# Optimization experiments

Hardware: AMD Instinct MI355X
Metric: run time of the kernel (lower is better)

The kernel has to match this reference:

```python
import jax, jax.numpy as jnp
import numpy as np
from jax import lax

DN = ('NCHW', 'OIHW', 'NCHW')

def binarize(w):
    # torch: w.sign().add(0.5).sign() maps w<0 -> -1, w>=0 -> +1 (0 -> +1)
    return jnp.where(w < 0, -1.0, 1.0).astype(w.dtype)

def bconv(x, w, b, dil):
    wb = binarize(w)
    y = lax.conv_general_dilated(x, wb, window_strides=(1, 1), padding='SAME',
                                 rhs_dilation=dil, dimension_numbers=DN)
    return y + b[None, :, None, None]

def setup_inputs() -> dict:
    key = jax.random.key(0)
    ks = jax.random.split(key, 9)
    C = 256
    Co = C // 4
    x = jax.random.normal(ks[0], (16, C, 128, 128), dtype=jnp.float32)
    w1 = jax.random.normal(ks[1], (Co, C, 1, 5), dtype=jnp.float32) * 0.05
    w2 = jax.random.normal(ks[2], (Co, C, 1, 5), dtype=jnp.float32) * 0.05
    w3 = jax.random.normal(ks[3], (Co, C, 5, 1), dtype=jnp.float32) * 0.05
    w4 = jax.random.normal(ks[4], (Co, C, 5, 1), dtype=jnp.float32) * 0.05
    b1 = jax.random.normal(ks[5], (Co,), dtype=jnp.float32) * 0.01
    b2 = jax.random.normal(ks[6], (Co,), dtype=jnp.float32) * 0.01
    b3 = jax.random.normal(ks[7], (Co,), dtype=jnp.float32) * 0.01
    b4 = jax.random.normal(ks[8], (Co,), dtype=jnp.float32) * 0.01
    return {'x': x, 'w1': w1, 'b1': b1, 'w2': w2, 'b2': b2,
            'w3': w3, 'b3': b3, 'w4': w4, 'b4': b4}

def reference(x, w1, b1, w2, b2, w3, b3, w4, b4):
    out1 = bconv(x, w1, b1, (1, 1))  # (1,5) dil 1
    out2 = bconv(x, w2, b2, (2, 2))  # (1,5) dil 2 (only W dim matters, H kernel=1)
    out3 = bconv(x, w3, b3, (1, 1))  # (5,1) dil 1
    out4 = bconv(x, w4, b4, (2, 2))  # (5,1) dil 2
    return jnp.concatenate([out1, out2, out3, out4], axis=1)
```

## Files before the change

kernel.cpp:

```cpp
#include <hip/hip_runtime.h>

typedef _Float16 half8  __attribute__((ext_vector_type(8)));
typedef float    floatx4 __attribute__((ext_vector_type(4)));

#define HW      128
#define CIN     256
#define NCHUNK  8
#define HALO_W  24
#define HALO_H  16
#define PITCH   20

__global__ void prep_weights(const float* __restrict__ w1,
                             const float* __restrict__ w2,
                             const float* __restrict__ w3,
                             const float* __restrict__ w4,
                             _Float16* __restrict__ wp)
{
    int idx  = blockIdx.x * 256 + threadIdx.x;
    int ci   = idx & 255;
    int rest = idx >> 8;
    int co   = rest & 63;
    int bt   = rest >> 6;
    int t    = bt % 5;
    int b    = bt / 5;
    const float* w = (b == 0) ? w1 : (b == 1) ? w2 : (b == 2) ? w3 : w4;
    float v = w[(co * 256 + ci) * 5 + t];
    wp[idx] = (v < 0.0f) ? (_Float16)(-1.0f) : (_Float16)(1.0f);
}

__global__ __launch_bounds__(256, 2)
void bconv_mfma(const float* __restrict__ x,
                const _Float16* __restrict__ wp,
                const float* __restrict__ bb1,
                const float* __restrict__ bb2,
                const float* __restrict__ bb3,
                const float* __restrict__ bb4,
                float* __restrict__ out)
{
    __shared__ __align__(16) unsigned int xs[HALO_H * HALO_W * PITCH];
    __shared__ float bias_s[256];

    const int tid  = threadIdx.x;
    const int w0t  = blockIdx.x * 16;
    const int h0t  = blockIdx.y * 8;
    const int nimg = blockIdx.z;

    {
        int br = tid >> 6, i = tid & 63;
        const float* bp = (br == 0) ? bb1 : (br == 1) ? bb2 : (br == 2) ? bb3 : bb4;
        bias_s[tid] = bp[i];
    }

    const int lane = tid & 63;
    const int wave = tid >> 6;
    const int quad = lane >> 4;
    const int wl   = lane & 15;

    floatx4 acc[4][8];
    #pragma unroll
    for (int m = 0; m < 4; ++m)
        #pragma unroll
        for (int n = 0; n < 8; ++n)
            acc[m][n] = (floatx4){0.f, 0.f, 0.f, 0.f};

    const int  dil   = (wave & 1) + 1;
    const bool horiz = (wave < 2);

    for (int chunk = 0; chunk < NCHUNK; ++chunk) {
        __syncthreads();

        #pragma unroll
        for (int s = 0; s < 6; ++s) {
            int u   = s * 256 + tid;
            int f   = u % 6;
            int g   = u / 6;
            int hh  = g & 15;
            int cp  = g >> 4;
            int ci0 = chunk * 32 + cp * 2;
            int hg  = h0t - 4 + hh;
            int wg  = w0t - 4 + f * 4;
            floatx4 v0 = {0.f,0.f,0.f,0.f}, v1 = {0.f,0.f,0.f,0.f};
            if (hg >= 0 && hg < HW && wg >= 0 && wg <= HW - 4) {
                const floatx4* p = (const floatx4*)(x + ((nimg * CIN + ci0) * HW + hg) * HW + wg);
                v0 = p[0];
                v1 = p[(HW * HW) / 4];
            }
            int pixb = hh * HALO_W + f * 4;
            #pragma unroll
            for (int i = 0; i < 4; ++i) {
                xs[(pixb + i) * PITCH + cp] =
                    __builtin_bit_cast(unsigned int,
                        __builtin_amdgcn_cvt_pkrtz(v0[i], v1[i]));
            }
        }
        __syncthreads();

        #pragma unroll
        for (int t = 0; t < 5; ++t) {
            half8 B[8];
            #pragma unroll
            for (int n = 0; n < 8; ++n) {
                int hh, ww;
                if (horiz) { hh = n + 4;                  ww = wl + 4 + (t - 2) * dil; }
                else       { hh = n + 4 + (t - 2) * dil;  ww = wl + 4; }
                B[n] = *(const half8*)&xs[(hh * HALO_W + ww) * PITCH + quad * 4];
            }
            #pragma unroll
            for (int m = 0; m < 4; ++m) {
                half8 A = *(const half8*)(wp +
                    (((wave * 5 + t) * 64 + m * 16 + wl) * 256 + chunk * 32 + quad * 8));
                #pragma unroll
                for (int n = 0; n < 8; ++n)
                    acc[m][n] = __builtin_amdgcn_mfma_f32_16x16x32_f16(A, B[n], acc[m][n], 0, 0, 0);
            }
        }
    }

    float bv[4][4];
    #pragma unroll
    for (int m = 0; m < 4; ++m)
        #pragma unroll
        for (int r = 0; r < 4; ++r)
            bv[m][r] = bias_s[wave * 64 + m * 16 + quad * 4 + r];

    #pragma unroll
    for (int m = 0; m < 4; ++m) {
        #pragma unroll
        for (int n = 0; n < 8; ++n) {
            int co   = wave * 64 + m * 16 + quad * 4;
            int base = ((nimg * 256 + co) * HW + (h0t + n)) * HW + w0t + wl;
            #pragma unroll
            for (int r = 0; r < 4; ++r)
                out[base + r * HW * HW] = acc[m][n][r] + bv[m][r];
        }
    }
}

extern "C" void kernel_launch(void* const* d_in, const int* in_sizes, int n_in,
                              void* d_out, int out_size, void* d_ws, size_t ws_size,
                              hipStream_t stream)
{
    (void)in_sizes; (void)n_in; (void)out_size; (void)ws_size;
    const float* x  = (const float*)d_in[0];
    const float* w1 = (const float*)d_in[1];
    const float* b1 = (const float*)d_in[2];
    const float* w2 = (const float*)d_in[3];
    const float* b2 = (const float*)d_in[4];
    const float* w3 = (const float*)d_in[5];
    const float* b3 = (const float*)d_in[6];
    const float* w4 = (const float*)d_in[7];
    const float* b4 = (const float*)d_in[8];
    float*    out = (float*)d_out;
    _Float16* wp  = (_Float16*)d_ws;

    prep_weights<<<1280, 256, 0, stream>>>(w1, w2, w3, w4, wp);

    dim3 grid(128 / 16, 128 / 8, 16);
    bconv_mfma<<<grid, dim3(256), 0, stream>>>(x, wp, b1, b2, b3, b4, out);
}
```

Baseline: 671.4 us.

## Double-buffer input halo in LDS and repack weights for coalesced loads

```diff
diff --git a/kernel.cpp b/kernel.cpp
--- a/kernel.cpp
+++ b/kernel.cpp
@@ -1,13 +1,15 @@
 #include <hip/hip_runtime.h>
 
-typedef _Float16 half8  __attribute__((ext_vector_type(8)));
+typedef _Float16 half8   __attribute__((ext_vector_type(8)));
 typedef float    floatx4 __attribute__((ext_vector_type(4)));
+typedef unsigned int uint4v __attribute__((ext_vector_type(4)));
 
 #define HW      128
 #define CIN     256
 #define NCHUNK  8
 #define HALO_W  24
 #define HALO_H  16
+#define NPIX    (HALO_W * HALO_H)
 #define PITCH   20
 
 __global__ void prep_weights(const float* __restrict__ w1,
@@ -17,13 +19,17 @@
                              _Float16* __restrict__ wp)
 {
     int idx  = blockIdx.x * 256 + threadIdx.x;
-    int ci   = idx & 255;
-    int rest = idx >> 8;
-    int co   = rest & 63;
-    int bt   = rest >> 6;
-    int t    = bt % 5;
-    int b    = bt / 5;
+    int j    = idx & 7;
+    int lane = (idx >> 3) & 63;
+    int m    = (idx >> 9) & 3;
+    int r3   = idx >> 11;
+    int t    = r3 % 5;
+    int r4   = r3 / 5;
+    int chunk= r4 & 7;
+    int b    = r4 >> 3;
     const float* w = (b == 0) ? w1 : (b == 1) ? w2 : (b == 2) ? w3 : w4;
+    int co = m * 16 + (lane & 15);
+    int ci = chunk * 32 + (lane >> 4) * 8 + j;
     float v = w[(co * 256 + ci) * 5 + t];
     wp[idx] = (v < 0.0f) ? (_Float16)(-1.0f) : (_Float16)(1.0f);
 }
@@ -37,7 +43,7 @@
                 const float* __restrict__ bb4,
                 float* __restrict__ out)
 {
-    __shared__ __align__(16) unsigned int xs[HALO_H * HALO_W * PITCH];
+    __shared__ __align__(16) unsigned int xs[2 * NPIX * PITCH];
     __shared__ float bias_s[256];
 
     const int tid  = threadIdx.x;
@@ -55,6 +61,8 @@
     const int wave = tid >> 6;
     const int quad = lane >> 4;
     const int wl   = lane & 15;
+    const int dil  = (wave & 1) + 1;
+    const bool horiz = (wave < 2);
 
     floatx4 acc[4][8];
     #pragma unroll
@@ -63,37 +71,40 @@
         for (int n = 0; n < 8; ++n)
             acc[m][n] = (floatx4){0.f, 0.f, 0.f, 0.f};
 
-    const int  dil   = (wave & 1) + 1;
-    const bool horiz = (wave < 2);
-
-    for (int chunk = 0; chunk < NCHUNK; ++chunk) {
-        __syncthreads();
-
+    auto stage = [&](int buf, int chunk) {
+        unsigned int* xb = &xs[buf * (NPIX * PITCH)];
         #pragma unroll
         for (int s = 0; s < 6; ++s) {
-            int u   = s * 256 + tid;
-            int f   = u % 6;
-            int g   = u / 6;
-            int hh  = g & 15;
-            int cp  = g >> 4;
-            int ci0 = chunk * 32 + cp * 2;
+            int idx = s * 256 + tid;
+            int hh  = idx / 96;
+            int rem = idx - hh * 96;
+            int cb  = rem / 24;
+            int ww  = rem - cb * 24;
             int hg  = h0t - 4 + hh;
-            int wg  = w0t - 4 + f * 4;
-            floatx4 v0 = {0.f,0.f,0.f,0.f}, v1 = {0.f,0.f,0.f,0.f};
-            if (hg >= 0 && hg < HW && wg >= 0 && wg <= HW - 4) {
-                const floatx4* p = (const floatx4*)(x + ((nimg * CIN + ci0) * HW + hg) * HW + wg);
-                v0 = p[0];
-                v1 = p[(HW * HW) / 4];
+            int wg  = w0t - 4 + ww;
+            float v[8];
+            #pragma unroll
+            for (int jj = 0; jj < 8; ++jj) v[jj] = 0.0f;
+            if (hg >= 0 && hg < HW && wg >= 0 && wg < HW) {
+                const float* p = x + (((nimg * CIN + chunk * 32 + cb * 8) * HW + hg) * HW + wg);
+                #pragma unroll
+                for (int jj = 0; jj < 8; ++jj) v[jj] = p[jj * HW * HW];
             }
-            int pixb = hh * HALO_W + f * 4;
+            uint4v u;
             #pragma unroll
-            for (int i = 0; i < 4; ++i) {
-                xs[(pixb + i) * PITCH + cp] =
-                    __builtin_bit_cast(unsigned int,
-                        __builtin_amdgcn_cvt_pkrtz(v0[i], v1[i]));
-            }
+            for (int jj = 0; jj < 4; ++jj)
+                u[jj] = __builtin_bit_cast(unsigned int,
+                            __builtin_amdgcn_cvt_pkrtz(v[2 * jj], v[2 * jj + 1]));
+            *(uint4v*)&xb[(hh * HALO_W + ww) * PITCH + cb * 4] = u;
         }
+    };
+
+    stage(0, 0);
+
+    for (int k = 0; k < NCHUNK; ++k) {
         __syncthreads();
+        const unsigned int* xb  = &xs[(k & 1) * (NPIX * PITCH)];
+        const _Float16*     wpc = wp + (wave * 8 + k) * (5 * 4 * 64 * 8);
 
         #pragma unroll
         for (int t = 0; t < 5; ++t) {
@@ -103,17 +114,18 @@
                 int hh, ww;
                 if (horiz) { hh = n + 4;                  ww = wl + 4 + (t - 2) * dil; }
                 else       { hh = n + 4 + (t - 2) * dil;  ww = wl + 4; }
-                B[n] = *(const half8*)&xs[(hh * HALO_W + ww) * PITCH + quad * 4];
+                B[n] = *(const half8*)&xb[(hh * HALO_W + ww) * PITCH + quad * 4];
             }
             #pragma unroll
             for (int m = 0; m < 4; ++m) {
-                half8 A = *(const half8*)(wp +
-                    (((wave * 5 + t) * 64 + m * 16 + wl) * 256 + chunk * 32 + quad * 8));
+                half8 A = *(const half8*)(wpc + ((t * 4 + m) * 64 + lane) * 8);
                 #pragma unroll
                 for (int n = 0; n < 8; ++n)
                     acc[m][n] = __builtin_amdgcn_mfma_f32_16x16x32_f16(A, B[n], acc[m][n], 0, 0, 0);
             }
         }
+
+        if (k + 1 < NCHUNK) stage((k + 1) & 1, k + 1);
     }
 
     float bv[4][4];
```

Result: no change. 660.8 us (-1.6%).
